# Kernel tuning notes

Hardware: AMD Instinct MI355X
Metric: run time of the kernel (lower is better)

The kernel has to match this reference:

```python
import jax, jax.numpy as jnp
import numpy as np

PATCH = 8      # patch_size
NFREQ = 8      # fourie_freq


def _fourier_feats(nH, nW, F, dtype):
    # Per-patch positional Fourier features: sin/cos of normalized patch-center
    # coords at F dyadic frequencies for both axes -> [nH, nW, 4F].
    iy = (jnp.arange(nH, dtype=jnp.float32) + 0.5) / nH
    ix = (jnp.arange(nW, dtype=jnp.float32) + 0.5) / nW
    freqs = (2.0 ** jnp.arange(F, dtype=jnp.float32)) * jnp.pi
    fy = iy[:, None] * freqs[None, :]  # [nH, F]
    fx = ix[:, None] * freqs[None, :]  # [nW, F]
    feats = jnp.concatenate([
        jnp.broadcast_to(jnp.sin(fy)[:, None, :], (nH, nW, F)),
        jnp.broadcast_to(jnp.cos(fy)[:, None, :], (nH, nW, F)),
        jnp.broadcast_to(jnp.sin(fx)[None, :, :], (nH, nW, F)),
        jnp.broadcast_to(jnp.cos(fx)[None, :, :], (nH, nW, F)),
    ], axis=-1)
    return feats.astype(dtype)


def setup_inputs() -> dict:
    key = jax.random.key(0)
    ks = jax.random.split(key, 5)
    B, C, H, W = 16, 64, 128, 128
    E, OC, P, F = 8, 64, PATCH, NFREQ
    GC = C + 4 * F  # gate_channel = 96
    x = jax.random.normal(ks[0], (B, C, H, W), jnp.float32)
    expert_w = jax.random.normal(ks[1], (E, OC, C, 3, 3), jnp.float32) * 0.05
    expert_b = jax.random.normal(ks[2], (E, OC), jnp.float32) * 0.05
    gate_w = jax.random.normal(ks[3], (E, GC * P * P), jnp.float32) * 0.02
    gate_b = jnp.zeros((E,), jnp.float32)
    return {"x": x, "expert_w": expert_w, "expert_b": expert_b,
            "gate_w": gate_w, "gate_b": gate_b}


def reference(x, expert_w, expert_b, gate_w, gate_b):
    B, C, H, W = x.shape
    E, OC = expert_w.shape[0], expert_w.shape[1]
    P, F = PATCH, NFREQ
    nH, nW = H // P, W // P

    # --- gating: per-patch softmax over experts ---
    # patches: [B, nH, nW, C, P, P] (matches nn.Flatten over (C,P,P))
    patches = x.reshape(B, C, nH, P, nW, P).transpose(0, 2, 4, 1, 3, 5)
    feats = _fourier_feats(nH, nW, F, x.dtype)                       # [nH,nW,4F]
    pos = jnp.broadcast_to(feats[None, :, :, :, None, None],
                           (B, nH, nW, 4 * F, P, P))
    gate_in = jnp.concatenate([patches, pos], axis=3).reshape(B, nH, nW, -1)
    logits = jnp.einsum('bhwf,ef->bhwe', gate_in, gate_w) + gate_b
    gate = jax.nn.softmax(logits, axis=-1)                           # [B,nH,nW,E]

    # --- experts: all E convs fused into a single conv, then gated combine ---
    wk = expert_w.reshape(E * OC, C, 3, 3)
    y = jax.lax.conv_general_dilated(
        x, wk, window_strides=(1, 1), padding='SAME',
        dimension_numbers=('NCHW', 'OIHW', 'NCHW'))
    y = y + expert_b.reshape(E * OC)[None, :, None, None]
    y = jax.nn.relu(y).reshape(B, E, OC, H, W)

    # upsample per-patch gates to pixel resolution: [B,E,H,W]
    g = gate.transpose(0, 3, 1, 2)                                   # [B,E,nH,nW]
    g = jnp.repeat(jnp.repeat(g, P, axis=2), P, axis=3)
    out = jnp.einsum('behw,bechw->bchw', g, y)                       # [B,OC,H,W]
    return out
```

## Files before the change

### kernel.cpp

```cpp
#include <hip/hip_runtime.h>

typedef short v8s __attribute__((ext_vector_type(8)));
typedef float v4f __attribute__((ext_vector_type(4)));

#define NCH    64
#define NHH    128
#define NWW    128
#define NOC    64
#define KSTEPS 18

#define COLS 34
#define SLAB_BYTES (6 * COLS * 128)
#define BBUF_OFF   SLAB_BYTES
#define NBUF 3
#define LDSG_OFF   (SLAB_BYTES + NBUF * 8192)
#define SMEM_BYTES (LDSG_OFF + 128)

#define GW_STRIDE 6144

__device__ __forceinline__ unsigned short f2bf(float f) {
  unsigned int u = __float_as_uint(f);
  u += 0x7FFFu + ((u >> 16) & 1u);
  return (unsigned short)(u >> 16);
}

__global__ void pack_b_kernel(const float* __restrict__ ew,
                              unsigned short* __restrict__ bp) {
  int f = blockIdx.x * 256 + threadIdx.x;
  int j = f & 7;
  int t = f >> 3;
  int lane = t & 63;
  t >>= 6;
  int nt = t & 3;
  t >>= 2;
  int s = t % KSTEPS;
  int e = t / KSTEPS;
  int k = s * 32 + (lane >> 4) * 8 + j;
  int n = nt * 16 + (lane & 15);
  int khw = k >> 6;
  int c = k & 63;
  bp[f] = f2bf(ew[((e * NOC + n) * NCH + c) * 9 + khw]);
}

__global__ __launch_bounds__(512) void gate_kernel(
    const float* __restrict__ x,
    const float* __restrict__ gw,
    const float* __restrict__ gb,
    float* __restrict__ gate_out) {
  __shared__ float xs[16][8][132];
  __shared__ float wsum[8][32];
  __shared__ float lg[16][8];

  const int pid = blockIdx.x;
  const int ph = pid & 15;
  const int b = pid >> 4;
  const int tid = threadIdx.x;
  const int e = tid >> 6;
  const int lane = tid & 63;

  if (tid < 256) {
    int e2 = tid >> 5, j = tid & 31;
    const float* p = gw + e2 * GW_STRIDE + 4096 + j * 64;
    float s = 0.f;
#pragma unroll
    for (int g = 0; g < 16; ++g) {
      float4 v = *(const float4*)(p + g * 4);
      s += v.x + v.y + v.z + v.w;
    }
    wsum[e2][j] = s;
  }

  float acc[16];
#pragma unroll
  for (int pw = 0; pw < 16; ++pw) acc[pw] = 0.f;

  const float* xrow = x + ((size_t)(b * NCH) * NHH + ph * 8) * NWW;

  for (int cc = 0; cc < 4; ++cc) {
    __syncthreads();
    for (int i = tid; i < 4096; i += 512) {
      int c = i >> 8;
      int py = (i >> 5) & 7;
      int w4 = i & 31;
      float4 v = *(const float4*)&xrow[(cc * 16 + c) * (NHH * NWW) + py * NWW + w4 * 4];
      *(float4*)&xs[c][py][w4 * 4] = v;
    }
    __syncthreads();
#pragma unroll
    for (int i = 0; i < 4; ++i) {
      int g = lane + 64 * i;
      int pxg = g & 1;
      int py = (g >> 1) & 7;
      int c = g >> 4;
      const float4 wv = *(const float4*)&gw[e * GW_STRIDE + (cc * 16 + c) * 64 + py * 8 + pxg * 4];
      const float* xp = &xs[c][py][pxg * 4];
#pragma unroll
      for (int pw = 0; pw < 16; ++pw) {
        float4 xv = *(const float4*)(xp + pw * 8);
        acc[pw] += xv.x * wv.x + xv.y * wv.y + xv.z * wv.z + xv.w * wv.w;
      }
    }
  }

#pragma unroll
  for (int pw = 0; pw < 16; ++pw) {
    float v = acc[pw];
#pragma unroll
    for (int off = 32; off > 0; off >>= 1) v += __shfl_xor(v, off, 64);
    if (lane == 0) lg[pw][e] = v;
  }
  __syncthreads();

  if (tid < 16) {
    const int pw = tid;
    const float cy = (ph + 0.5f) / 16.0f;
    const float cx = (pw + 0.5f) / 16.0f;
    float l[8];
#pragma unroll
    for (int ee = 0; ee < 8; ++ee) l[ee] = lg[pw][ee] + gb[ee];
    for (int j = 0; j < 32; ++j) {
      float freq = (float)(1 << (j & 7)) * 3.14159265358979323846f;
      float base = (j < 16) ? cy : cx;
      float a = base * freq;
      float v = ((j >> 3) & 1) ? cosf(a) : sinf(a);
#pragma unroll
      for (int ee = 0; ee < 8; ++ee) l[ee] += v * wsum[ee][j];
    }
    float mx = -1e30f;
#pragma unroll
    for (int ee = 0; ee < 8; ++ee) mx = fmaxf(mx, l[ee]);
    float sum = 0.f;
#pragma unroll
    for (int ee = 0; ee < 8; ++ee) { l[ee] = expf(l[ee] - mx); sum += l[ee]; }
    float inv = 1.0f / sum;
#pragma unroll
    for (int ee = 0; ee < 8; ++ee)
      gate_out[(pid * 16 + pw) * 8 + ee] = l[ee] * inv;
  }
}

__device__ __forceinline__ void load_stage(const unsigned short* __restrict__ bp,
                                           char* smem, int gs, int buf,
                                           int wid, int lane) {
  const char* gsrc = (const char*)bp + gs * 8192 + wid * 2048 + lane * 16;
  char* ldst = smem + BBUF_OFF + buf * 8192 + wid * 2048;
  __builtin_amdgcn_global_load_lds(
      (const __attribute__((address_space(1))) void*)gsrc,
      (__attribute__((address_space(3))) void*)ldst, 16, 0, 0);
  __builtin_amdgcn_global_load_lds(
      (const __attribute__((address_space(1))) void*)(gsrc + 1024),
      (__attribute__((address_space(3))) void*)(ldst + 1024), 16, 0, 0);
}

__global__ __launch_bounds__(256, 3) void moe_conv_kernel(
    const float* __restrict__ x,
    const float* __restrict__ eb,
    const unsigned short* __restrict__ bp,
    const float* __restrict__ gate,
    float* __restrict__ out) {
  __shared__ __align__(16) char smem[SMEM_BYTES];
  unsigned short* bbufs = (unsigned short*)(smem + BBUF_OFF);
  float* ldsg = (float*)(smem + LDSG_OFF);

  const int tid = threadIdx.x;
  const int bid = blockIdx.x;
  const int wseg = bid & 3;
  const int hq = (bid >> 2) & 31;
  const int b = bid >> 7;
  const int w0 = wseg * 32;
  const int wid = tid >> 6;
  const int lane = tid & 63;
  const int quad = lane >> 4;
  const int l15 = lane & 15;

  load_stage(bp, smem, 0, 0, wid, lane);

  if (tid < 32) {
    ldsg[tid] = gate[((b * 16 + (hq >> 1)) * 16 + wseg * 4 + (tid >> 3)) * 8 + (tid & 7)];
  }

  const int hbase = hq * 4 - 1;
  const int wbase = w0 - 1;
  for (int flat = tid; flat < 6 * 32 * COLS; flat += 256) {
    int col = flat % COLS;
    int t = flat / COLS;
    int cp = t & 31;
    int r = t >> 5;
    int gh = hbase + r;
    int gw_ = wbase + col;
    float v0 = 0.f, v1 = 0.f;
    if (((unsigned)gh < 128u) && ((unsigned)gw_ < 128u)) {
      const float* px = x + (((b * NCH + cp * 2) * NHH + gh) * NWW + gw_);
      v0 = px[0];
      v1 = px[NHH * NWW];
    }
    unsigned int pk = (unsigned int)f2bf(v0) | ((unsigned int)f2bf(v1) << 16);
    int srow = r * COLS + col;
    int boff = ((cp * 4) + ((srow & 7) << 4)) & 127;
    *(unsigned int*)(smem + srow * 128 + boff) = pk;
  }

  load_stage(bp, smem, 1, 1, wid, lane);
  __syncthreads();

  const v4f vzero = {0.f, 0.f, 0.f, 0.f};
  v4f oacc[2][4];
#pragma unroll
  for (int mt = 0; mt < 2; ++mt)
#pragma unroll
    for (int nt = 0; nt < 4; ++nt) oacc[mt][nt] = vzero;

  const int q16 = quad * 16;
  const int lw  = l15 + 2 * wid;
  const int rowb = (wid * COLS + l15) * 128;

  for (int e = 0; e < 8; ++e) {
    v4f vacc[2][4];
#pragma unroll
    for (int mt = 0; mt < 2; ++mt)
#pragma unroll
      for (int nt = 0; nt < 4; ++nt) vacc[mt][nt] = vzero;

#pragma unroll
    for (int st = 0; st < 9; ++st) {
      const int gs = e * 9 + st;
      if (gs > 0) {
        asm volatile("s_waitcnt vmcnt(2)" ::: "memory");
        __builtin_amdgcn_s_barrier();
        __builtin_amdgcn_sched_barrier(0);
      }
      {
        const int g2 = gs + 2;
        const int gsrc = (g2 < 72) ? g2 : 71;
        load_stage(bp, smem, gsrc, (st + 2) % 3, wid, lane);
      }

      const unsigned short* bstage = bbufs + (st % 3) * 4096;
#pragma unroll
      for (int sub = 0; sub < 2; ++sub) {
        const int sl = st * 2 + sub;
        const int kh = sl / 6;
        const int kw = (sl / 2) % 3;
        const int ch = sl & 1;
        v8s bf[4];
#pragma unroll
        for (int nt = 0; nt < 4; ++nt)
          bf[nt] = *(const v8s*)(bstage + (sub * 4 + nt) * 512 + lane * 8);
        const int rot = ((lw + 2 * kh + kw) & 7) << 4;
        const int aoff = (q16 + ch * 64 + rot) & 127;
        const char* arow = smem + rowb + (kh * COLS + kw) * 128 + aoff;
        __builtin_amdgcn_s_setprio(1);
#pragma unroll
        for (int mt = 0; mt < 2; ++mt) {
          const v8s a = *(const v8s*)(arow + mt * 2048);
#pragma unroll
          for (int nt = 0; nt < 4; ++nt)
            vacc[mt][nt] = __builtin_amdgcn_mfma_f32_16x16x32_bf16(a, bf[nt], vacc[mt][nt], 0, 0, 0);
        }
        __builtin_amdgcn_s_setprio(0);
      }
    }

    float bias[4];
#pragma unroll
    for (int nt = 0; nt < 4; ++nt) bias[nt] = eb[e * NOC + nt * 16 + l15];
#pragma unroll
    for (int mt = 0; mt < 2; ++mt) {
      float g = ldsg[(mt * 2 + (quad >> 1)) * 8 + e];
#pragma unroll
      for (int nt = 0; nt < 4; ++nt)
#pragma unroll
        for (int r = 0; r < 4; ++r) {
          float v = fmaxf(vacc[mt][nt][r] + bias[nt], 0.f);
          oacc[mt][nt][r] += v * g;
        }
    }
  }

  __syncthreads();
  float* tb = (float*)smem + wid * 2304;
#pragma unroll
  for (int mt = 0; mt < 2; ++mt)
#pragma unroll
    for (int nt = 0; nt < 4; ++nt)
      *(v4f*)(tb + (nt * 16 + l15) * 36 + mt * 16 + quad * 4) = oacc[mt][nt];

  const int h = hq * 4 + wid;
  const int l7 = lane & 7;
  const int o8 = lane >> 3;
#pragma unroll
  for (int g4 = 0; g4 < 8; ++g4) {
    const int ocl = g4 * 8 + o8;
    const v4f vv = *(const v4f*)(tb + ocl * 36 + l7 * 4);
    float* dst = out + ((b * NOC + ocl) * NHH + h) * NWW + w0 + l7 * 4;
    *(v4f*)dst = vv;
  }
}

extern "C" void kernel_launch(void* const* d_in, const int* in_sizes, int n_in,
                              void* d_out, int out_size, void* d_ws, size_t ws_size,
                              hipStream_t stream) {
  const float* x  = (const float*)d_in[0];
  const float* ew = (const float*)d_in[1];
  const float* eb = (const float*)d_in[2];
  const float* gw = (const float*)d_in[3];
  const float* gb = (const float*)d_in[4];
  float* out = (float*)d_out;

  unsigned short* bp = (unsigned short*)d_ws;
  float* gate = (float*)((char*)d_ws + 589824);

  hipLaunchKernelGGL(pack_b_kernel, dim3(1152), dim3(256), 0, stream, ew, bp);
  hipLaunchKernelGGL(gate_kernel, dim3(256), dim3(512), 0, stream, x, gw, gb, gate);
  hipLaunchKernelGGL(moe_conv_kernel, dim3(2048), dim3(256), 0, stream, x, eb, bp, gate, out);
}
```

Baseline: 280.2 us.

## Split experts across wave pairs so each wave reuses B fragments over four row tiles

Reorders the packed expert weights so each pipeline stage holds one K-slice for two experts. Each pair of waves now covers two output rows, with one wave handling experts 0-3 and the other 4-7, so every B fragment load feeds four A tiles instead of two. The two waves' partial gated outputs are combined through shared memory, which adds a barrier. Register use doubles (16 accumulators for vacc and oacc each), so launch bounds drop to 2 blocks per SM, trading occupancy for fewer LDS B reads per MFMA.

```diff
diff --git a/kernel.cpp b/kernel.cpp
--- a/kernel.cpp
+++ b/kernel.cpp
@@ -33,9 +33,12 @@
   t >>= 6;
   int nt = t & 3;
   t >>= 2;
-  int s = t % KSTEPS;
-  int e = t / KSTEPS;
-  int k = s * 32 + (lane >> 4) * 8 + j;
+  int e01 = t & 1;
+  int gs = t >> 1;
+  int sl = gs % KSTEPS;
+  int g = gs / KSTEPS;
+  int e = g + 4 * e01;
+  int k = sl * 32 + (lane >> 4) * 8 + j;
   int n = nt * 16 + (lane & 15);
   int khw = k >> 6;
   int c = k & 63;
@@ -152,7 +155,7 @@
       (__attribute__((address_space(3))) void*)(ldst + 1024), 16, 0, 0);
 }
 
-__global__ __launch_bounds__(256, 3) void moe_conv_kernel(
+__global__ __launch_bounds__(256, 2) void moe_conv_kernel(
     const float* __restrict__ x,
     const float* __restrict__ eb,
     const unsigned short* __restrict__ bp,
@@ -172,6 +175,8 @@
   const int lane = tid & 63;
   const int quad = lane >> 4;
   const int l15 = lane & 15;
+  const int rp = wid >> 1;
+  const int eh = wid & 1;
 
   load_stage(bp, smem, 0, 0, wid, lane);
 
@@ -204,86 +209,110 @@
   __syncthreads();
 
   const v4f vzero = {0.f, 0.f, 0.f, 0.f};
-  v4f oacc[2][4];
-#pragma unroll
-  for (int mt = 0; mt < 2; ++mt)
-#pragma unroll
-    for (int nt = 0; nt < 4; ++nt) oacc[mt][nt] = vzero;
+  v4f oacc[4][4];
+#pragma unroll
+  for (int m = 0; m < 4; ++m)
+#pragma unroll
+    for (int nt = 0; nt < 4; ++nt) oacc[m][nt] = vzero;
 
   const int q16 = quad * 16;
-  const int lw  = l15 + 2 * wid;
-  const int rowb = (wid * COLS + l15) * 128;
-
-  for (int e = 0; e < 8; ++e) {
-    v4f vacc[2][4];
-#pragma unroll
-    for (int mt = 0; mt < 2; ++mt)
-#pragma unroll
-      for (int nt = 0; nt < 4; ++nt) vacc[mt][nt] = vzero;
-
-#pragma unroll
-    for (int st = 0; st < 9; ++st) {
-      const int gs = e * 9 + st;
+  const int s7 = 4 * rp + l15;
+  const int rowb0 = ((rp * 2 + 0) * COLS + l15) * 128;
+  const int rowb1 = ((rp * 2 + 1) * COLS + l15) * 128;
+
+  for (int g = 0; g < 4; ++g) {
+    v4f vacc[4][4];
+#pragma unroll
+    for (int m = 0; m < 4; ++m)
+#pragma unroll
+      for (int nt = 0; nt < 4; ++nt) vacc[m][nt] = vzero;
+
+#pragma unroll
+    for (int sl = 0; sl < KSTEPS; ++sl) {
+      const int gs = g * KSTEPS + sl;
       if (gs > 0) {
         asm volatile("s_waitcnt vmcnt(2)" ::: "memory");
         __builtin_amdgcn_s_barrier();
         __builtin_amdgcn_sched_barrier(0);
       }
       {
-        const int g2 = gs + 2;
-        const int gsrc = (g2 < 72) ? g2 : 71;
-        load_stage(bp, smem, gsrc, (st + 2) % 3, wid, lane);
-      }
-
-      const unsigned short* bstage = bbufs + (st % 3) * 4096;
-#pragma unroll
-      for (int sub = 0; sub < 2; ++sub) {
-        const int sl = st * 2 + sub;
-        const int kh = sl / 6;
-        const int kw = (sl / 2) % 3;
-        const int ch = sl & 1;
-        v8s bf[4];
-#pragma unroll
-        for (int nt = 0; nt < 4; ++nt)
-          bf[nt] = *(const v8s*)(bstage + (sub * 4 + nt) * 512 + lane * 8);
-        const int rot = ((lw + 2 * kh + kw) & 7) << 4;
+        int g2 = gs + 2;
+        if (g2 > 71) g2 = 71;
+        load_stage(bp, smem, g2, (gs + 2) % 3, wid, lane);
+      }
+
+      const unsigned short* bstage = bbufs + (gs % 3) * 4096;
+      const int kh = sl / 6;
+      const int kw = (sl / 2) % 3;
+      const int ch = sl & 1;
+      v8s bf[4];
+#pragma unroll
+      for (int nt = 0; nt < 4; ++nt)
+        bf[nt] = *(const v8s*)(bstage + (eh * 4 + nt) * 512 + lane * 8);
+      const int kbyte = (kh * COLS + kw) * 128;
+      __builtin_amdgcn_s_setprio(1);
+#pragma unroll
+      for (int r01 = 0; r01 < 2; ++r01) {
+        const int rot = ((s7 + 2 * (r01 + kh) + kw) & 7) << 4;
         const int aoff = (q16 + ch * 64 + rot) & 127;
-        const char* arow = smem + rowb + (kh * COLS + kw) * 128 + aoff;
-        __builtin_amdgcn_s_setprio(1);
-#pragma unroll
-        for (int mt = 0; mt < 2; ++mt) {
-          const v8s a = *(const v8s*)(arow + mt * 2048);
+        const int rbase = (r01 ? rowb1 : rowb0) + kbyte + aoff;
+#pragma unroll
+        for (int ct = 0; ct < 2; ++ct) {
+          const v8s a = *(const v8s*)(smem + rbase + ct * 2048);
 #pragma unroll
           for (int nt = 0; nt < 4; ++nt)
-            vacc[mt][nt] = __builtin_amdgcn_mfma_f32_16x16x32_bf16(a, bf[nt], vacc[mt][nt], 0, 0, 0);
+            vacc[r01 * 2 + ct][nt] =
+                __builtin_amdgcn_mfma_f32_16x16x32_bf16(a, bf[nt], vacc[r01 * 2 + ct][nt], 0, 0, 0);
         }
-        __builtin_amdgcn_s_setprio(0);
-      }
-    }
-
+      }
+      __builtin_amdgcn_s_setprio(0);
+    }
+
+    const int e = g + 4 * eh;
     float bias[4];
 #pragma unroll
     for (int nt = 0; nt < 4; ++nt) bias[nt] = eb[e * NOC + nt * 16 + l15];
 #pragma unroll
-    for (int mt = 0; mt < 2; ++mt) {
-      float g = ldsg[(mt * 2 + (quad >> 1)) * 8 + e];
+    for (int m = 0; m < 4; ++m) {
+      const int ct = m & 1;
+      float gv = ldsg[(ct * 2 + (quad >> 1)) * 8 + e];
 #pragma unroll
       for (int nt = 0; nt < 4; ++nt)
 #pragma unroll
         for (int r = 0; r < 4; ++r) {
-          float v = fmaxf(vacc[mt][nt][r] + bias[nt], 0.f);
-          oacc[mt][nt][r] += v * g;
+          float v = fmaxf(vacc[m][nt][r] + bias[nt], 0.f);
+          oacc[m][nt][r] += v * gv;
         }
     }
   }
 
   __syncthreads();
-  float* tb = (float*)smem + wid * 2304;
-#pragma unroll
-  for (int mt = 0; mt < 2; ++mt)
-#pragma unroll
-    for (int nt = 0; nt < 4; ++nt)
-      *(v4f*)(tb + (nt * 16 + l15) * 36 + mt * 16 + quad * 4) = oacc[mt][nt];
+  float* tbf = (float*)smem;
+  if (eh == 0) {
+#pragma unroll
+    for (int m = 0; m < 4; ++m) {
+      const int r01 = m >> 1, ct = m & 1;
+#pragma unroll
+      for (int nt = 0; nt < 4; ++nt)
+        *(v4f*)(tbf + ((rp * 2 + r01) * 64 + nt * 16 + l15) * 36 + ct * 16 + quad * 4) =
+            oacc[m][nt];
+    }
+  }
+  __syncthreads();
+  if (eh == 1) {
+#pragma unroll
+    for (int m = 0; m < 4; ++m) {
+      const int r01 = m >> 1, ct = m & 1;
+#pragma unroll
+      for (int nt = 0; nt < 4; ++nt) {
+        float* p = tbf + ((rp * 2 + r01) * 64 + nt * 16 + l15) * 36 + ct * 16 + quad * 4;
+        v4f t = *(v4f*)p;
+        t += oacc[m][nt];
+        *(v4f*)p = t;
+      }
+    }
+  }
+  __syncthreads();
 
   const int h = hq * 4 + wid;
   const int l7 = lane & 7;
@@ -291,7 +320,7 @@
 #pragma unroll
   for (int g4 = 0; g4 < 8; ++g4) {
     const int ocl = g4 * 8 + o8;
-    const v4f vv = *(const v4f*)(tb + ocl * 36 + l7 * 4);
+    const v4f vv = *(const v4f*)(tbf + (wid * 64 + ocl) * 36 + l7 * 4);
     float* dst = out + ((b * NOC + ocl) * NHH + h) * NWW + w0 + l7 * 4;
     *(v4f*)dst = vv;
   }
```

Result: no change. 282.1 us (+0.7%).
